# Kernel tuning notes

Measured on AMD Instinct MI355X. Metric: run time of the kernel, lower is better.

## Reference

```python
import jax, jax.numpy as jnp
import numpy as np

N_NODES = 100000
N_EDGES = 600000


def gcn_conv(x, W, b, src, dst, ew):
    """PyG GCNConv with edge weights: sym-normalized A-hat (self loops weight 1), then +bias."""
    n = x.shape[0]
    # degree includes self-loop weight 1.0
    deg = jnp.zeros((n,), x.dtype).at[dst].add(ew) + 1.0
    dinv = jax.lax.rsqrt(deg)                      # deg > 0 always (self loop)
    norm = dinv[src] * ew * dinv[dst]              # [E]
    h = x @ W                                      # [n, out]
    agg = jax.ops.segment_sum(h[src] * norm[:, None], dst, num_segments=n)
    agg = agg + h * (dinv * dinv)[:, None]         # self-loop contribution (weight 1)
    return agg + b


def setup_inputs() -> dict:
    key = jax.random.key(0)
    ks = jax.random.split(key, 16)
    x = jax.random.normal(ks[0], (N_NODES, 8), dtype=jnp.float32)
    edge_index = jax.random.randint(ks[1], (2, N_EDGES), 0, N_NODES, dtype=jnp.int32)
    edge_weight = jax.random.uniform(ks[2], (N_EDGES,), dtype=jnp.float32)
    batch = jnp.zeros((N_NODES,), dtype=jnp.int32)  # single graph
    C2ER = jax.random.normal(ks[3], (4,), dtype=jnp.float32)

    def lin(k, fan_in, fan_out):
        kw, kb = jax.random.split(k)
        s = 1.0 / np.sqrt(fan_in)
        W = jax.random.uniform(kw, (fan_in, fan_out), jnp.float32, -s, s)
        b = jax.random.uniform(kb, (fan_out,), jnp.float32, -s, s)
        return W, b

    W1, b1 = lin(ks[4], 8, 32)
    W2, b2 = lin(ks[5], 32, 128)
    W3, b3 = lin(ks[6], 128, 128)
    W4, b4 = lin(ks[7], 128, 32)
    L1W, L1b = lin(ks[8], 68, 128)
    L2W, L2b = lin(ks[9], 128, 128)
    L3W, L3b = lin(ks[10], 128, 10)
    return dict(x=x, edge_index=edge_index, edge_weight=edge_weight, batch=batch, C2ER=C2ER,
                W1=W1, b1=b1, W2=W2, b2=b2, W3=W3, b3=b3, W4=W4, b4=b4,
                L1W=L1W, L1b=L1b, L2W=L2W, L2b=L2b, L3W=L3W, L3b=L3b)


def reference(x, edge_index, edge_weight, batch, C2ER,
              W1, b1, W2, b2, W3, b3, W4, b4,
              L1W, L1b, L2W, L2b, L3W, L3b):
    src, dst = edge_index[0], edge_index[1]
    # dropout is inference-mode identity
    h = jax.nn.relu(gcn_conv(x, W1, b1, src, dst, edge_weight))
    x0 = jax.ops.segment_max(h, batch, num_segments=1)          # [1, 32]
    h = jax.nn.relu(gcn_conv(h, W2, b2, src, dst, edge_weight))
    h = jax.nn.relu(gcn_conv(h, W3, b3, src, dst, edge_weight))
    h = jax.nn.relu(gcn_conv(h, W4, b4, src, dst, edge_weight))
    x1 = jax.ops.segment_max(h, batch, num_segments=1)          # [1, 32]
    code = jnp.concatenate([x0, x1, C2ER.reshape(1, 4)], axis=1)  # [1, 68]
    z = jax.nn.relu(code @ L1W + L1b)
    z = jax.nn.relu(z @ L2W + L2b)
    out = jax.nn.softmax(z @ L3W + L3b, axis=1)                  # [1, 10]
    return out, code
```

## Files before the change

### kernel.cpp

```cpp
#include <hip/hip_runtime.h>
#include <hip/hip_bf16.h>

#define NN 100000
#define NE 600000
#define PAD 40

using bf16 = __hip_bfloat16;
typedef float f32x4 __attribute__((ext_vector_type(4)));
typedef short s16x8 __attribute__((ext_vector_type(8)));
typedef unsigned int u32x2 __attribute__((ext_vector_type(2)));
typedef unsigned int u32x4 __attribute__((ext_vector_type(4)));

__device__ __forceinline__ float bu2f(unsigned int u16) {
    union { float f; unsigned int i; } c; c.i = u16 << 16; return c.f;
}
__device__ __forceinline__ unsigned int f2bu(float f) {
    bf16 h = __float2bfloat16(f);
    return (unsigned int)*reinterpret_cast<unsigned short*>(&h);
}
__device__ __forceinline__ u32x2 st4bf(float4 a) {
    u32x2 u;
    u.x = f2bu(a.x) | (f2bu(a.y) << 16);
    u.y = f2bu(a.z) | (f2bu(a.w) << 16);
    return u;
}
__device__ __forceinline__ void up8(uint4 u, float* a) {
    a[0] = bu2f(u.x & 0xffffu); a[1] = bu2f(u.x >> 16);
    a[2] = bu2f(u.y & 0xffffu); a[3] = bu2f(u.y >> 16);
    a[4] = bu2f(u.z & 0xffffu); a[5] = bu2f(u.z >> 16);
    a[6] = bu2f(u.w & 0xffffu); a[7] = bu2f(u.w >> 16);
}
__device__ __forceinline__ int rec_src(unsigned int r) { return (int)(r >> 15); }
__device__ __forceinline__ float rec_w(unsigned int r) { return bu2f(r & 0x7fffu); }

__global__ void k_prep(int* cnt, float* x0x1,
                       const float* W2, const float* W3, const float* W4,
                       short* Wt2, short* Wt3, short* Wt4) {
    int i = blockIdx.x * 256 + threadIdx.x;
    if (i < NN) cnt[i] = 0;
    if (i < 64) x0x1[i] = 0.0f;
    if (i < 4096) {
        int n = i >> 5, k = i & 31;
        Wt2[n * 32 + k] = (short)f2bu(W2[k * 128 + n]);
    }
    if (i >= 4096 && i < 20480) {
        int j = i - 4096; int n = j >> 7, k = j & 127;
        Wt3[n * 128 + k] = (short)f2bu(W3[k * 128 + n]);
    }
    if (i >= 20480 && i < 24576) {
        int j = i - 20480; int n = j >> 7, k = j & 127;
        Wt4[n * 128 + k] = (short)f2bu(W4[k * 32 + n]);
    }
}

__global__ void k_fill(const int* srcI, const int* dstI, const float* ew,
                       int* cnt, unsigned int* edges) {
    int e = blockIdx.x * 256 + threadIdx.x;
    if (e >= NE) return;
    int d = dstI[e];
    int r = atomicAdd(&cnt[d], 1);
    if (r < PAD)
        edges[(size_t)d * PAD + r] = ((unsigned int)srcI[e] << 15) | (f2bu(ew[e]) & 0x7fffu);
}

__global__ void k_deg(int* cnt, unsigned int* edges, float* dinv,
                      const float* x, float* xs) {
    int n = blockIdx.x * 256 + threadIdx.x;
    if (n >= NN) return;
    int len = cnt[n];
    if (len > PAD) { len = PAD; cnt[n] = PAD; }
    unsigned int* row = edges + (size_t)n * PAD;
    int lenr = (len + 3) & ~3;
    if (lenr < 12) lenr = 12;
    for (int i = len; i < lenr; i++) row[i] = 0;
    float s = 1.0f;
    for (int i = 0; i < len; i++) s += rec_w(row[i]);
    float di = rsqrtf(s);
    dinv[n] = di;
    const float4* x4 = (const float4*)x;
    float4 a = x4[(size_t)n * 2], b = x4[(size_t)n * 2 + 1];
    a.x *= di; a.y *= di; a.z *= di; a.w *= di;
    b.x *= di; b.y *= di; b.z *= di; b.w *= di;
    ((float4*)xs)[(size_t)n * 2] = a;
    ((float4*)xs)[(size_t)n * 2 + 1] = b;
}

__global__ __launch_bounds__(256) void k_ag8(const float* __restrict__ xs,
        const float* __restrict__ dinv, const int* __restrict__ cnt,
        const unsigned int* __restrict__ edges, float* __restrict__ outF) {
    int tid = blockIdx.x * 256 + threadIdx.x;
    int n = tid >> 1, g = tid & 1;
    if (n >= NN) return;
    const float4* h4 = (const float4*)xs;
    float4 acc = h4[(size_t)n * 2 + g];
    int len = cnt[n];
    const uint4* row4 = (const uint4*)(edges + (size_t)n * PAD);
    uint4 r0 = row4[0], r1 = row4[1], r2 = row4[2];
    unsigned int rec[12] = {r0.x, r0.y, r0.z, r0.w, r1.x, r1.y, r1.z, r1.w,
                            r2.x, r2.y, r2.z, r2.w};
    float4 gg[12];
#pragma unroll
    for (int e = 0; e < 12; e++) gg[e] = h4[(size_t)rec_src(rec[e]) * 2 + g];
#pragma unroll
    for (int e = 0; e < 12; e++) {
        float w = rec_w(rec[e]);
        acc.x = fmaf(w, gg[e].x, acc.x); acc.y = fmaf(w, gg[e].y, acc.y);
        acc.z = fmaf(w, gg[e].z, acc.z); acc.w = fmaf(w, gg[e].w, acc.w);
    }
    int lenq = (len + 3) >> 2;
    for (int q = 3; q < lenq; q++) {
        uint4 rr = row4[q];
        float4 v0 = h4[(size_t)rec_src(rr.x) * 2 + g];
        float4 v1 = h4[(size_t)rec_src(rr.y) * 2 + g];
        float4 v2 = h4[(size_t)rec_src(rr.z) * 2 + g];
        float4 v3 = h4[(size_t)rec_src(rr.w) * 2 + g];
        float w0 = rec_w(rr.x), w1 = rec_w(rr.y), w2 = rec_w(rr.z), w3 = rec_w(rr.w);
        acc.x = fmaf(w0, v0.x, acc.x); acc.y = fmaf(w0, v0.y, acc.y);
        acc.z = fmaf(w0, v0.z, acc.z); acc.w = fmaf(w0, v0.w, acc.w);
        acc.x = fmaf(w1, v1.x, acc.x); acc.y = fmaf(w1, v1.y, acc.y);
        acc.z = fmaf(w1, v1.z, acc.z); acc.w = fmaf(w1, v1.w, acc.w);
        acc.x = fmaf(w2, v2.x, acc.x); acc.y = fmaf(w2, v2.y, acc.y);
        acc.z = fmaf(w2, v2.z, acc.z); acc.w = fmaf(w2, v2.w, acc.w);
        acc.x = fmaf(w3, v3.x, acc.x); acc.y = fmaf(w3, v3.y, acc.y);
        acc.z = fmaf(w3, v3.z, acc.z); acc.w = fmaf(w3, v3.w, acc.w);
    }
    float dn = dinv[n];
    acc.x *= dn; acc.y *= dn; acc.z *= dn; acc.w *= dn;
    ((float4*)outF)[(size_t)n * 2 + g] = acc;
}

__global__ __launch_bounds__(256) void k_gemm8(const float* __restrict__ hin,
                                               const float* __restrict__ Wf,
                                               const float* __restrict__ dinv,
                                               unsigned int* __restrict__ hW,
                                               const float* __restrict__ bias,
                                               float* xmax) {
    __shared__ float xs[256 * 12];
    __shared__ int smax[32];
    const int base = blockIdx.x * 256;
    const int t = threadIdx.x;
#pragma unroll
    for (int i = 0; i < 2; i++) {
        int idx = t + 256 * i;
        int row = idx >> 1, k4 = idx & 1;
        int node = base + row;
        if (node >= NN) node = NN - 1;
        float4 v = ((const float4*)hin)[(size_t)node * 2 + k4];
        *(float4*)&xs[row * 12 + 4 * k4] = v;
    }
    if (t < 32) smax[t] = 0;
    __syncthreads();
    const int cg = t & 7, ng = t >> 3;
    float4 acc[8];
#pragma unroll
    for (int i = 0; i < 8; i++) acc[i] = make_float4(0.f, 0.f, 0.f, 0.f);
    const float4* wr = (const float4*)Wf;
#pragma unroll
    for (int k = 0; k < 8; k++) {
        float4 w = wr[k * 8 + cg];
#pragma unroll
        for (int i = 0; i < 8; i++) {
            float xv = xs[(ng * 8 + i) * 12 + k];
            acc[i].x = fmaf(xv, w.x, acc[i].x);
            acc[i].y = fmaf(xv, w.y, acc[i].y);
            acc[i].z = fmaf(xv, w.z, acc[i].z);
            acc[i].w = fmaf(xv, w.w, acc[i].w);
        }
    }
    float4 bb = ((const float4*)bias)[cg];
    float4 mx = make_float4(0.f, 0.f, 0.f, 0.f);
#pragma unroll
    for (int i = 0; i < 8; i++) {
        int node = base + ng * 8 + i;
        acc[i].x = fmaxf(acc[i].x + bb.x, 0.f);
        acc[i].y = fmaxf(acc[i].y + bb.y, 0.f);
        acc[i].z = fmaxf(acc[i].z + bb.z, 0.f);
        acc[i].w = fmaxf(acc[i].w + bb.w, 0.f);
        mx.x = fmaxf(mx.x, acc[i].x); mx.y = fmaxf(mx.y, acc[i].y);
        mx.z = fmaxf(mx.z, acc[i].z); mx.w = fmaxf(mx.w, acc[i].w);
        if (node < NN) {
            float dn = dinv[node];
            float4 sc = make_float4(acc[i].x * dn, acc[i].y * dn, acc[i].z * dn, acc[i].w * dn);
            ((u32x2*)hW)[(size_t)node * 8 + cg] = st4bf(sc);
        }
    }
    atomicMax(&smax[cg * 4 + 0], __float_as_int(mx.x));
    atomicMax(&smax[cg * 4 + 1], __float_as_int(mx.y));
    atomicMax(&smax[cg * 4 + 2], __float_as_int(mx.z));
    atomicMax(&smax[cg * 4 + 3], __float_as_int(mx.w));
    __syncthreads();
    if (t < 32) atomicMax((int*)&xmax[t], smax[t]);
}

__global__ __launch_bounds__(256) void k_f2b(const uint4* __restrict__ hs1,
        const float* __restrict__ dinv, const int* __restrict__ cnt,
        const unsigned int* __restrict__ edges, const short* __restrict__ Wt2,
        const short* __restrict__ Wt3, const float* __restrict__ b2,
        unsigned short* __restrict__ T) {
    __shared__ short xs[64 * 40];
    __shared__ short hs[64 * 136];
    const int base = blockIdx.x * 64;
    const int t = threadIdx.x;
    {
        int nl = t >> 2, c = t & 3;
        int n = base + nl;
        float acc[8] = {0.f, 0.f, 0.f, 0.f, 0.f, 0.f, 0.f, 0.f};
        if (n < NN) {
            float a[8];
            up8(hs1[(size_t)n * 4 + c], a);
#pragma unroll
            for (int j = 0; j < 8; j++) acc[j] = a[j];
            int len = cnt[n];
            const uint4* row4 = (const uint4*)(edges + (size_t)n * PAD);
            uint4 r0 = row4[0], r1 = row4[1], r2 = row4[2];
            unsigned int rec[12] = {r0.x, r0.y, r0.z, r0.w, r1.x, r1.y, r1.z, r1.w,
                                    r2.x, r2.y, r2.z, r2.w};
            uint4 gg[12];
#pragma unroll
            for (int e = 0; e < 12; e++) gg[e] = hs1[(size_t)rec_src(rec[e]) * 4 + c];
#pragma unroll
            for (int e = 0; e < 12; e++) {
                float w = rec_w(rec[e]);
                float a0[8];
                up8(gg[e], a0);
#pragma unroll
                for (int j = 0; j < 8; j++) acc[j] = fmaf(w, a0[j], acc[j]);
            }
            int lenq = (len + 3) >> 2;
            for (int q = 3; q < lenq; q++) {
                uint4 rr = row4[q];
                uint4 u0 = hs1[(size_t)rec_src(rr.x) * 4 + c];
                uint4 u1 = hs1[(size_t)rec_src(rr.y) * 4 + c];
                uint4 u2 = hs1[(size_t)rec_src(rr.z) * 4 + c];
                uint4 u3 = hs1[(size_t)rec_src(rr.w) * 4 + c];
                float w0 = rec_w(rr.x), w1 = rec_w(rr.y);
                float w2 = rec_w(rr.z), w3 = rec_w(rr.w);
                float a0[8];
                up8(u0, a0);
#pragma unroll
                for (int j = 0; j < 8; j++) acc[j] = fmaf(w0, a0[j], acc[j]);
                up8(u1, a0);
#pragma unroll
                for (int j = 0; j < 8; j++) acc[j] = fmaf(w1, a0[j], acc[j]);
                up8(u2, a0);
#pragma unroll
                for (int j = 0; j < 8; j++) acc[j] = fmaf(w2, a0[j], acc[j]);
                up8(u3, a0);
#pragma unroll
                for (int j = 0; j < 8; j++) acc[j] = fmaf(w3, a0[j], acc[j]);
            }
            float dn = dinv[n];
#pragma unroll
            for (int j = 0; j < 8; j++) acc[j] *= dn;
        }
        unsigned int p[4];
        p[0] = f2bu(acc[0]) | (f2bu(acc[1]) << 16);
        p[1] = f2bu(acc[2]) | (f2bu(acc[3]) << 16);
        p[2] = f2bu(acc[4]) | (f2bu(acc[5]) << 16);
        p[3] = f2bu(acc[6]) | (f2bu(acc[7]) << 16);
        *(uint4*)&xs[nl * 40 + c * 8] = make_uint4(p[0], p[1], p[2], p[3]);
    }
    __syncthreads();
    const int wave = t >> 6;
    const int lane = t & 63;
    const int m = lane & 15, quad = lane >> 4;
    {
        s16x8 a = *(const s16x8*)&xs[(wave * 16 + m) * 40 + quad * 8];
        f32x4 acc[8];
#pragma unroll
        for (int nt = 0; nt < 8; nt++) {
            s16x8 b = *(const s16x8*)(Wt2 + (size_t)(nt * 16 + m) * 32 + quad * 8);
            acc[nt] = (f32x4){0.f, 0.f, 0.f, 0.f};
            acc[nt] = __builtin_amdgcn_mfma_f32_16x16x32_bf16(a, b, acc[nt], 0, 0, 0);
        }
#pragma unroll
        for (int nt = 0; nt < 8; nt++) {
            float bb = b2[nt * 16 + m];
#pragma unroll
            for (int r = 0; r < 4; r++) {
                int row = wave * 16 + quad * 4 + r;
                float v = fmaxf(acc[nt][r] + bb, 0.f);
                hs[row * 136 + nt * 16 + m] = (short)f2bu(v);
            }
        }
    }
    __syncthreads();
    {
        s16x8 a2[4];
#pragma unroll
        for (int s = 0; s < 4; s++)
            a2[s] = *(const s16x8*)&hs[(wave * 16 + m) * 136 + s * 32 + quad * 8];
        f32x4 acc[8];
#pragma unroll
        for (int nt = 0; nt < 8; nt++) acc[nt] = (f32x4){0.f, 0.f, 0.f, 0.f};
#pragma unroll
        for (int s = 0; s < 4; s++) {
            s16x8 b[8];
#pragma unroll
            for (int nt = 0; nt < 8; nt++)
                b[nt] = *(const s16x8*)(Wt3 + ((size_t)(nt * 16 + m) * 128 + s * 32 + quad * 8));
#pragma unroll
            for (int nt = 0; nt < 8; nt++)
                acc[nt] = __builtin_amdgcn_mfma_f32_16x16x32_bf16(a2[s], b[nt], acc[nt], 0, 0, 0);
        }
        const int orl = wave * 16 + quad * 4;
        float dsc[4];
#pragma unroll
        for (int r = 0; r < 4; r++) {
            int nd = base + orl + r;
            dsc[r] = (nd < NN) ? dinv[nd] : 1.0f;
        }
#pragma unroll
        for (int nt = 0; nt < 8; nt++) {
#pragma unroll
            for (int r = 0; r < 4; r++)
                hs[(orl + r) * 136 + nt * 16 + m] = (short)f2bu(acc[nt][r] * dsc[r]);
        }
        __builtin_amdgcn_s_waitcnt(0);
        int nl = wave * 16 + (lane >> 2);
        int node = base + nl;
        if (node < NN) {
#pragma unroll
            for (int j = 0; j < 4; j++) {
                int cs = (lane & 3) * 32 + j * 8;
                *(uint4*)(T + (size_t)node * 128 + cs) = *(const uint4*)&hs[nl * 136 + cs];
            }
        }
    }
}

__global__ __launch_bounds__(256) void k_agW4(const uint4* __restrict__ hin,
        const float* __restrict__ dinv, const int* __restrict__ cnt,
        const unsigned int* __restrict__ edges, const float* __restrict__ bias,
        const short* __restrict__ Wt4, unsigned short* __restrict__ Out) {
    __shared__ short ht[16 * 136];
    const int base = blockIdx.x * 16;
    const int t = threadIdx.x;
    int nl = t >> 4, c = t & 15;
    int n = base + nl;
    float acc[8];
    bool valid = (n < NN);
    if (valid) {
        float a[8];
        up8(hin[(size_t)n * 16 + c], a);
#pragma unroll
        for (int j = 0; j < 8; j++) acc[j] = a[j];
        int len = cnt[n];
        const uint4* row4 = (const uint4*)(edges + (size_t)n * PAD);
        uint4 r0 = row4[0], r1 = row4[1], r2 = row4[2];
        unsigned int rec[12] = {r0.x, r0.y, r0.z, r0.w, r1.x, r1.y, r1.z, r1.w,
                                r2.x, r2.y, r2.z, r2.w};
        uint4 gg[12];
#pragma unroll
        for (int e = 0; e < 12; e++) gg[e] = hin[(size_t)rec_src(rec[e]) * 16 + c];
#pragma unroll
        for (int e = 0; e < 12; e++) {
            float w = rec_w(rec[e]);
            float a0[8];
            up8(gg[e], a0);
#pragma unroll
            for (int j = 0; j < 8; j++) acc[j] = fmaf(w, a0[j], acc[j]);
        }
        int lenq = (len + 3) >> 2;
        for (int q = 3; q < lenq; q++) {
            uint4 rr = row4[q];
            uint4 u0 = hin[(size_t)rec_src(rr.x) * 16 + c];
            uint4 u1 = hin[(size_t)rec_src(rr.y) * 16 + c];
            uint4 u2 = hin[(size_t)rec_src(rr.z) * 16 + c];
            uint4 u3 = hin[(size_t)rec_src(rr.w) * 16 + c];
            float w0 = rec_w(rr.x), w1 = rec_w(rr.y);
            float w2 = rec_w(rr.z), w3 = rec_w(rr.w);
            float a0[8];
            up8(u0, a0);
#pragma unroll
            for (int j = 0; j < 8; j++) acc[j] = fmaf(w0, a0[j], acc[j]);
            up8(u1, a0);
#pragma unroll
            for (int j = 0; j < 8; j++) acc[j] = fmaf(w1, a0[j], acc[j]);
            up8(u2, a0);
#pragma unroll
            for (int j = 0; j < 8; j++) acc[j] = fmaf(w2, a0[j], acc[j]);
            up8(u3, a0);
#pragma unroll
            for (int j = 0; j < 8; j++) acc[j] = fmaf(w3, a0[j], acc[j]);
        }
        float dn = dinv[n];
#pragma unroll
        for (int j = 0; j < 8; j++)
            acc[j] = fmaxf(fmaf(dn, acc[j], bias[c * 8 + j]), 0.f);
    } else {
#pragma unroll
        for (int j = 0; j < 8; j++) acc[j] = 0.f;
    }
    {
        uint4 o;
        o.x = f2bu(acc[0]) | (f2bu(acc[1]) << 16);
        o.y = f2bu(acc[2]) | (f2bu(acc[3]) << 16);
        o.z = f2bu(acc[4]) | (f2bu(acc[5]) << 16);
        o.w = f2bu(acc[6]) | (f2bu(acc[7]) << 16);
        *(uint4*)&ht[nl * 136 + c * 8] = o;
    }
    __syncthreads();
    if (t < 64) {
        const int lane = t;
        const int m = lane & 15, quad = lane >> 4;
        s16x8 a[4];
#pragma unroll
        for (int s = 0; s < 4; s++)
            a[s] = *(const s16x8*)&ht[m * 136 + s * 32 + quad * 8];
        f32x4 acc2[2];
#pragma unroll
        for (int nt = 0; nt < 2; nt++) acc2[nt] = (f32x4){0.f, 0.f, 0.f, 0.f};
#pragma unroll
        for (int s = 0; s < 4; s++) {
#pragma unroll
            for (int nt = 0; nt < 2; nt++) {
                s16x8 b = *(const s16x8*)(Wt4 + ((size_t)(nt * 16 + m) * 128 + s * 32 + quad * 8));
                acc2[nt] = __builtin_amdgcn_mfma_f32_16x16x32_bf16(a[s], b, acc2[nt], 0, 0, 0);
            }
        }
        float dsc[4];
#pragma unroll
        for (int r = 0; r < 4; r++) {
            int nd = base + quad * 4 + r;
            dsc[r] = (nd < NN) ? dinv[nd] : 0.f;
        }
#pragma unroll
        for (int nt = 0; nt < 2; nt++) {
#pragma unroll
            for (int r = 0; r < 4; r++)
                ht[(quad * 4 + r) * 136 + nt * 16 + m] = (short)f2bu(acc2[nt][r] * dsc[r]);
        }
        __builtin_amdgcn_s_waitcnt(0);
        int nl2 = lane >> 2, ch = lane & 3;
        int node = base + nl2;
        if (node < NN)
            *(uint4*)(Out + (size_t)node * 32 + ch * 8) = *(const uint4*)&ht[nl2 * 136 + ch * 8];
    }
}

template<int W, int EPI>
__global__ __launch_bounds__(256) void k_ag16(const uint4* __restrict__ hin,
        const float* __restrict__ dinv, const int* __restrict__ cnt,
        const unsigned int* __restrict__ edges, const float* __restrict__ bias,
        uint4* __restrict__ outB, float* __restrict__ xmax) {
    constexpr int TPN = W / 8;
    __shared__ int smax[(EPI == 3) ? W : 1];
    int tid = blockIdx.x * 256 + threadIdx.x;
    int n = tid / TPN, c = tid % TPN;
    if (EPI == 3) {
        if (threadIdx.x < W) smax[threadIdx.x] = 0;
        __syncthreads();
    }
    float acc[8];
    bool valid = (n < NN);
    if (valid) {
        float a[8];
        up8(hin[(size_t)n * TPN + c], a);
#pragma unroll
        for (int j = 0; j < 8; j++) acc[j] = a[j];
        int len = cnt[n];
        const uint4* row4 = (const uint4*)(edges + (size_t)n * PAD);
        uint4 r0 = row4[0], r1 = row4[1], r2 = row4[2];
        unsigned int rec[12] = {r0.x, r0.y, r0.z, r0.w, r1.x, r1.y, r1.z, r1.w,
                                r2.x, r2.y, r2.z, r2.w};
        uint4 gg[12];
#pragma unroll
        for (int e = 0; e < 12; e++) gg[e] = hin[(size_t)rec_src(rec[e]) * TPN + c];
#pragma unroll
        for (int e = 0; e < 12; e++) {
            float w = rec_w(rec[e]);
            float a0[8];
            up8(gg[e], a0);
#pragma unroll
            for (int j = 0; j < 8; j++) acc[j] = fmaf(w, a0[j], acc[j]);
        }
        int lenq = (len + 3) >> 2;
        for (int q = 3; q < lenq; q++) {
            uint4 rr = row4[q];
            uint4 u0 = hin[(size_t)rec_src(rr.x) * TPN + c];
            uint4 u1 = hin[(size_t)rec_src(rr.y) * TPN + c];
            uint4 u2 = hin[(size_t)rec_src(rr.z) * TPN + c];
            uint4 u3 = hin[(size_t)rec_src(rr.w) * TPN + c];
            float w0 = rec_w(rr.x), w1 = rec_w(rr.y);
            float w2 = rec_w(rr.z), w3 = rec_w(rr.w);
            float a0[8];
            up8(u0, a0);
#pragma unroll
            for (int j = 0; j < 8; j++) acc[j] = fmaf(w0, a0[j], acc[j]);
            up8(u1, a0);
#pragma unroll
            for (int j = 0; j < 8; j++) acc[j] = fmaf(w1, a0[j], acc[j]);
            up8(u2, a0);
#pragma unroll
            for (int j = 0; j < 8; j++) acc[j] = fmaf(w2, a0[j], acc[j]);
            up8(u3, a0);
#pragma unroll
            for (int j = 0; j < 8; j++) acc[j] = fmaf(w3, a0[j], acc[j]);
        }
        float dn = dinv[n];
#pragma unroll
        for (int j = 0; j < 8; j++)
            acc[j] = fmaxf(fmaf(dn, acc[j], bias[c * 8 + j]), 0.f);
        if (EPI == 1) {
            uint4 o;
            o.x = f2bu(acc[0]) | (f2bu(acc[1]) << 16);
            o.y = f2bu(acc[2]) | (f2bu(acc[3]) << 16);
            o.z = f2bu(acc[4]) | (f2bu(acc[5]) << 16);
            o.w = f2bu(acc[6]) | (f2bu(acc[7]) << 16);
            outB[(size_t)n * TPN + c] = o;
        } else {
#pragma unroll
            for (int j = 0; j < 8; j++) atomicMax(&smax[c * 8 + j], __float_as_int(acc[j]));
        }
    }
    if (EPI == 3) {
        __syncthreads();
        if (threadIdx.x < W) atomicMax((int*)&xmax[threadIdx.x], smax[threadIdx.x]);
    }
}

__global__ void k_mlp(const float* x0x1, const float* C2,
                      const float* L1W, const float* L1b,
                      const float* L2W, const float* L2b,
                      const float* L3W, const float* L3b, float* out) {
    __shared__ float code[68], z1[128], z2[128];
    int t = threadIdx.x;
    if (t < 64) code[t] = x0x1[t];
    else if (t < 68) code[t] = C2[t - 64];
    __syncthreads();
    float acc = L1b[t];
    for (int i = 0; i < 68; i++) acc = fmaf(code[i], L1W[i * 128 + t], acc);
    z1[t] = fmaxf(acc, 0.f);
    __syncthreads();
    acc = L2b[t];
    for (int i = 0; i < 128; i++) acc = fmaf(z1[i], L2W[i * 128 + t], acc);
    z2[t] = fmaxf(acc, 0.f);
    __syncthreads();
    if (t == 0) {
        float lg[10];
        for (int c = 0; c < 10; c++) {
            float a = L3b[c];
            for (int i = 0; i < 128; i++) a = fmaf(z2[i], L3W[i * 10 + c], a);
            lg[c] = a;
        }
        float m = lg[0];
        for (int c = 1; c < 10; c++) m = fmaxf(m, lg[c]);
        float s = 0.f;
        for (int c = 0; c < 10; c++) { lg[c] = __expf(lg[c] - m); s += lg[c]; }
        float inv = 1.f / s;
        for (int c = 0; c < 10; c++) out[c] = lg[c] * inv;
    }
    if (t < 68) out[10 + t] = code[t];
}

extern "C" void kernel_launch(void* const* d_in, const int* in_sizes, int n_in,
                              void* d_out, int out_size, void* d_ws, size_t ws_size,
                              hipStream_t stream) {
    const float* x   = (const float*)d_in[0];
    const int*   ei  = (const int*)d_in[1];
    const float* ew  = (const float*)d_in[2];
    const float* C2  = (const float*)d_in[4];
    const float* W1  = (const float*)d_in[5],  * b1 = (const float*)d_in[6];
    const float* W2  = (const float*)d_in[7],  * b2 = (const float*)d_in[8];
    const float* W3  = (const float*)d_in[9],  * b3 = (const float*)d_in[10];
    const float* W4  = (const float*)d_in[11], * b4 = (const float*)d_in[12];
    const float* L1W = (const float*)d_in[13], * L1b = (const float*)d_in[14];
    const float* L2W = (const float*)d_in[15], * L2b = (const float*)d_in[16];
    const float* L3W = (const float*)d_in[17], * L3b = (const float*)d_in[18];
    float* out = (float*)d_out;
    (void)in_sizes; (void)n_in; (void)out_size; (void)ws_size;

    const size_t szF = (size_t)NN * 128 * 4;
    char* p = (char*)d_ws;
    char* H       = p;          p += szF;
    char* T       = p;          p += szF;
    unsigned int* edges = (unsigned int*)p; p += (size_t)NN * PAD * 4;
    float* dinv   = (float*)p;  p += (size_t)NN * 4;
    int*   cnt    = (int*)p;    p += (size_t)NN * 4;
    float* xs     = (float*)p;  p += (size_t)NN * 8 * 4;
    float* x0x1   = (float*)p;  p += 256 * 4;
    short* Wt2    = (short*)p;  p += 4096 * 2;
    short* Wt3    = (short*)p;  p += 16384 * 2;
    short* Wt4    = (short*)p;  p += 4096 * 2;

    const int* srcI = ei;
    const int* dstI = ei + NE;

    dim3 B(256);
    k_prep<<<dim3((NN + 255) / 256), B, 0, stream>>>(cnt, x0x1, W2, W3, W4, Wt2, Wt3, Wt4);
    k_fill<<<dim3((NE + 255) / 256), B, 0, stream>>>(srcI, dstI, ew, cnt, edges);
    k_deg<<<dim3((NN + 255) / 256), B, 0, stream>>>(cnt, edges, dinv, x, xs);

    k_ag8<<<dim3((NN * 2 + 255) / 256), B, 0, stream>>>(xs, dinv, cnt, edges, (float*)T);
    k_gemm8<<<dim3((NN + 255) / 256), B, 0, stream>>>((const float*)T, W1, dinv, (unsigned int*)H, b1, x0x1);
    k_f2b<<<dim3((NN + 63) / 64), B, 0, stream>>>(
        (const uint4*)H, dinv, cnt, edges, Wt2, Wt3, b2, (unsigned short*)T);
    k_agW4<<<dim3((NN + 15) / 16), B, 0, stream>>>(
        (const uint4*)T, dinv, cnt, edges, b3, Wt4, (unsigned short*)H);
    k_ag16<32, 3><<<dim3((NN * 4 + 255) / 256), B, 0, stream>>>(
        (const uint4*)H, dinv, cnt, edges, b4, nullptr, x0x1 + 32);

    k_mlp<<<dim3(1), dim3(128), 0, stream>>>(x0x1, C2, L1W, L1b, L2W, L2b, L3W, L3b, out);
}
```

Before: 275.4 us.

## Shrink k_f2b blocks to 16 nodes, split gather and MFMA columns across waves

```diff
diff --git a/kernel.cpp b/kernel.cpp
--- a/kernel.cpp
+++ b/kernel.cpp
@@ -29,6 +29,10 @@
     a[2] = bu2f(u.y & 0xffffu); a[3] = bu2f(u.y >> 16);
     a[4] = bu2f(u.z & 0xffffu); a[5] = bu2f(u.z >> 16);
     a[6] = bu2f(u.w & 0xffffu); a[7] = bu2f(u.w >> 16);
+}
+__device__ __forceinline__ void up4(uint2 u, float* a) {
+    a[0] = bu2f(u.x & 0xffffu); a[1] = bu2f(u.x >> 16);
+    a[2] = bu2f(u.y & 0xffffu); a[3] = bu2f(u.y >> 16);
 }
 __device__ __forceinline__ int rec_src(unsigned int r) { return (int)(r >> 15); }
 __device__ __forceinline__ float rec_w(unsigned int r) { return bu2f(r & 0x7fffu); }
@@ -192,94 +196,95 @@
     if (t < 32) atomicMax((int*)&xmax[t], smax[t]);
 }
 
-__global__ __launch_bounds__(256) void k_f2b(const uint4* __restrict__ hs1,
+__global__ __launch_bounds__(128) void k_f2b(const unsigned int* __restrict__ hs1,
         const float* __restrict__ dinv, const int* __restrict__ cnt,
         const unsigned int* __restrict__ edges, const short* __restrict__ Wt2,
         const short* __restrict__ Wt3, const float* __restrict__ b2,
         unsigned short* __restrict__ T) {
-    __shared__ short xs[64 * 40];
-    __shared__ short hs[64 * 136];
-    const int base = blockIdx.x * 64;
+    __shared__ short xs[16 * 40];
+    __shared__ short hs[16 * 136];
+    const int base = blockIdx.x * 16;
     const int t = threadIdx.x;
     {
-        int nl = t >> 2, c = t & 3;
+        int nl = t >> 3, c = t & 7;
         int n = base + nl;
-        float acc[8] = {0.f, 0.f, 0.f, 0.f, 0.f, 0.f, 0.f, 0.f};
+        float acc[4] = {0.f, 0.f, 0.f, 0.f};
         if (n < NN) {
-            float a[8];
-            up8(hs1[(size_t)n * 4 + c], a);
-#pragma unroll
-            for (int j = 0; j < 8; j++) acc[j] = a[j];
+            const uint2* h2v = (const uint2*)hs1;
+            float a[4];
+            up4(h2v[(size_t)n * 8 + c], a);
+#pragma unroll
+            for (int j = 0; j < 4; j++) acc[j] = a[j];
             int len = cnt[n];
             const uint4* row4 = (const uint4*)(edges + (size_t)n * PAD);
             uint4 r0 = row4[0], r1 = row4[1], r2 = row4[2];
             unsigned int rec[12] = {r0.x, r0.y, r0.z, r0.w, r1.x, r1.y, r1.z, r1.w,
                                     r2.x, r2.y, r2.z, r2.w};
-            uint4 gg[12];
-#pragma unroll
-            for (int e = 0; e < 12; e++) gg[e] = hs1[(size_t)rec_src(rec[e]) * 4 + c];
+            uint2 gg[12];
+#pragma unroll
+            for (int e = 0; e < 12; e++) gg[e] = h2v[(size_t)rec_src(rec[e]) * 8 + c];
 #pragma unroll
             for (int e = 0; e < 12; e++) {
                 float w = rec_w(rec[e]);
-                float a0[8];
-                up8(gg[e], a0);
-#pragma unroll
-                for (int j = 0; j < 8; j++) acc[j] = fmaf(w, a0[j], acc[j]);
+                float a0[4];
+                up4(gg[e], a0);
+#pragma unroll
+                for (int j = 0; j < 4; j++) acc[j] = fmaf(w, a0[j], acc[j]);
             }
             int lenq = (len + 3) >> 2;
             for (int q = 3; q < lenq; q++) {
                 uint4 rr = row4[q];
-                uint4 u0 = hs1[(size_t)rec_src(rr.x) * 4 + c];
-                uint4 u1 = hs1[(size_t)rec_src(rr.y) * 4 + c];
-                uint4 u2 = hs1[(size_t)rec_src(rr.z) * 4 + c];
-                uint4 u3 = hs1[(size_t)rec_src(rr.w) * 4 + c];
+                uint2 u0 = h2v[(size_t)rec_src(rr.x) * 8 + c];
+                uint2 u1 = h2v[(size_t)rec_src(rr.y) * 8 + c];
+                uint2 u2 = h2v[(size_t)rec_src(rr.z) * 8 + c];
+                uint2 u3 = h2v[(size_t)rec_src(rr.w) * 8 + c];
                 float w0 = rec_w(rr.x), w1 = rec_w(rr.y);
                 float w2 = rec_w(rr.z), w3 = rec_w(rr.w);
-                float a0[8];
-                up8(u0, a0);
-#pragma unroll
-                for (int j = 0; j < 8; j++) acc[j] = fmaf(w0, a0[j], acc[j]);
-                up8(u1, a0);
-#pragma unroll
-                for (int j = 0; j < 8; j++) acc[j] = fmaf(w1, a0[j], acc[j]);
-                up8(u2, a0);
-#pragma unroll
-                for (int j = 0; j < 8; j++) acc[j] = fmaf(w2, a0[j], acc[j]);
-                up8(u3, a0);
-#pragma unroll
-                for (int j = 0; j < 8; j++) acc[j] = fmaf(w3, a0[j], acc[j]);
+                float a0[4];
+                up4(u0, a0);
+#pragma unroll
+                for (int j = 0; j < 4; j++) acc[j] = fmaf(w0, a0[j], acc[j]);
+                up4(u1, a0);
+#pragma unroll
+                for (int j = 0; j < 4; j++) acc[j] = fmaf(w1, a0[j], acc[j]);
+                up4(u2, a0);
+#pragma unroll
+                for (int j = 0; j < 4; j++) acc[j] = fmaf(w2, a0[j], acc[j]);
+                up4(u3, a0);
+#pragma unroll
+                for (int j = 0; j < 4; j++) acc[j] = fmaf(w3, a0[j], acc[j]);
             }
             float dn = dinv[n];
 #pragma unroll
-            for (int j = 0; j < 8; j++) acc[j] *= dn;
-        }
-        unsigned int p[4];
-        p[0] = f2bu(acc[0]) | (f2bu(acc[1]) << 16);
-        p[1] = f2bu(acc[2]) | (f2bu(acc[3]) << 16);
-        p[2] = f2bu(acc[4]) | (f2bu(acc[5]) << 16);
-        p[3] = f2bu(acc[6]) | (f2bu(acc[7]) << 16);
-        *(uint4*)&xs[nl * 40 + c * 8] = make_uint4(p[0], p[1], p[2], p[3]);
+            for (int j = 0; j < 4; j++) acc[j] *= dn;
+        }
+        u32x2 p;
+        p.x = f2bu(acc[0]) | (f2bu(acc[1]) << 16);
+        p.y = f2bu(acc[2]) | (f2bu(acc[3]) << 16);
+        *(u32x2*)&xs[nl * 40 + c * 4] = p;
     }
     __syncthreads();
     const int wave = t >> 6;
     const int lane = t & 63;
     const int m = lane & 15, quad = lane >> 4;
     {
-        s16x8 a = *(const s16x8*)&xs[(wave * 16 + m) * 40 + quad * 8];
-        f32x4 acc[8];
-#pragma unroll
-        for (int nt = 0; nt < 8; nt++) {
+        s16x8 a = *(const s16x8*)&xs[m * 40 + quad * 8];
+        f32x4 acc[4];
+#pragma unroll
+        for (int i = 0; i < 4; i++) {
+            int nt = wave * 4 + i;
             s16x8 b = *(const s16x8*)(Wt2 + (size_t)(nt * 16 + m) * 32 + quad * 8);
-            acc[nt] = (f32x4){0.f, 0.f, 0.f, 0.f};
-            acc[nt] = __builtin_amdgcn_mfma_f32_16x16x32_bf16(a, b, acc[nt], 0, 0, 0);
-        }
-#pragma unroll
-        for (int nt = 0; nt < 8; nt++) {
+            acc[i] = (f32x4){0.f, 0.f, 0.f, 0.f};
+            acc[i] = __builtin_amdgcn_mfma_f32_16x16x32_bf16(a, b, acc[i], 0, 0, 0);
+        }
+#pragma unroll
+        for (int i = 0; i < 4; i++) {
+            int nt = wave * 4 + i;
             float bb = b2[nt * 16 + m];
 #pragma unroll
             for (int r = 0; r < 4; r++) {
-                int row = wave * 16 + quad * 4 + r;
-                float v = fmaxf(acc[nt][r] + bb, 0.f);
+                int row = quad * 4 + r;
+                float v = fmaxf(acc[i][r] + bb, 0.f);
                 hs[row * 136 + nt * 16 + m] = (short)f2bu(v);
             }
         }
@@ -289,42 +294,40 @@
         s16x8 a2[4];
 #pragma unroll
         for (int s = 0; s < 4; s++)
-            a2[s] = *(const s16x8*)&hs[(wave * 16 + m) * 136 + s * 32 + quad * 8];
-        f32x4 acc[8];
-#pragma unroll
-        for (int nt = 0; nt < 8; nt++) acc[nt] = (f32x4){0.f, 0.f, 0.f, 0.f};
+            a2[s] = *(const s16x8*)&hs[m * 136 + s * 32 + quad * 8];
+        __syncthreads();
+        f32x4 acc[4];
+#pragma unroll
+        for (int i = 0; i < 4; i++) acc[i] = (f32x4){0.f, 0.f, 0.f, 0.f};
 #pragma unroll
         for (int s = 0; s < 4; s++) {
-            s16x8 b[8];
-#pragma unroll
-            for (int nt = 0; nt < 8; nt++)
-                b[nt] = *(const s16x8*)(Wt3 + ((size_t)(nt * 16 + m) * 128 + s * 32 + quad * 8));
-#pragma unroll
-            for (int nt = 0; nt < 8; nt++)
-                acc[nt] = __builtin_amdgcn_mfma_f32_16x16x32_bf16(a2[s], b[nt], acc[nt], 0, 0, 0);
-        }
-        const int orl = wave * 16 + quad * 4;
+#pragma unroll
+            for (int i = 0; i < 4; i++) {
+                int nt = wave * 4 + i;
+                s16x8 b = *(const s16x8*)(Wt3 + ((size_t)(nt * 16 + m) * 128 + s * 32 + quad * 8));
+                acc[i] = __builtin_amdgcn_mfma_f32_16x16x32_bf16(a2[s], b, acc[i], 0, 0, 0);
+            }
+        }
         float dsc[4];
 #pragma unroll
         for (int r = 0; r < 4; r++) {
-            int nd = base + orl + r;
+            int nd = base + quad * 4 + r;
             dsc[r] = (nd < NN) ? dinv[nd] : 1.0f;
         }
 #pragma unroll
-        for (int nt = 0; nt < 8; nt++) {
+        for (int i = 0; i < 4; i++) {
+            int nt = wave * 4 + i;
 #pragma unroll
             for (int r = 0; r < 4; r++)
-                hs[(orl + r) * 136 + nt * 16 + m] = (short)f2bu(acc[nt][r] * dsc[r]);
+                hs[(quad * 4 + r) * 136 + nt * 16 + m] = (short)f2bu(acc[i][r] * dsc[r]);
         }
         __builtin_amdgcn_s_waitcnt(0);
-        int nl = wave * 16 + (lane >> 2);
+        int nl = lane >> 2, ch = lane & 3;
         int node = base + nl;
         if (node < NN) {
-#pragma unroll
-            for (int j = 0; j < 4; j++) {
-                int cs = (lane & 3) * 32 + j * 8;
-                *(uint4*)(T + (size_t)node * 128 + cs) = *(const uint4*)&hs[nl * 136 + cs];
-            }
+            int cs = wave * 64 + ch * 16;
+            *(uint4*)(T + (size_t)node * 128 + cs) = *(const uint4*)&hs[nl * 136 + cs];
+            *(uint4*)(T + (size_t)node * 128 + cs + 8) = *(const uint4*)&hs[nl * 136 + cs + 8];
         }
     }
 }
@@ -594,8 +597,8 @@
 
     k_ag8<<<dim3((NN * 2 + 255) / 256), B, 0, stream>>>(xs, dinv, cnt, edges, (float*)T);
     k_gemm8<<<dim3((NN + 255) / 256), B, 0, stream>>>((const float*)T, W1, dinv, (unsigned int*)H, b1, x0x1);
-    k_f2b<<<dim3((NN + 63) / 64), B, 0, stream>>>(
-        (const uint4*)H, dinv, cnt, edges, Wt2, Wt3, b2, (unsigned short*)T);
+    k_f2b<<<dim3((NN + 15) / 16), dim3(128), 0, stream>>>(
+        (const unsigned int*)H, dinv, cnt, edges, Wt2, Wt3, b2, (unsigned short*)T);
     k_agW4<<<dim3((NN + 15) / 16), B, 0, stream>>>(
         (const uint4*)T, dinv, cnt, edges, b3, Wt4, (unsigned short*)H);
     k_ag16<32, 3><<<dim3((NN * 4 + 255) / 256), B, 0, stream>>>(
```

Result: faster. 268.8 us (median of 2 runs) (-2.4%).
